# Kernel optimization log

Hardware: AMD Instinct MI355X
Metric: run time of the kernel (lower is better)

## Reference

```python
import jax, jax.numpy as jnp
import numpy as np


def setup_inputs() -> dict:
    key = jax.random.key(0)
    ks = jax.random.split(key, 6)
    B, N1, N2 = 4, 16384, 4096
    C1, C2 = 128, 256
    H1, H2 = 256, 128
    Cin = C1 + C2  # 384
    return {
        "xyz1": jax.random.normal(ks[0], (B, N1, 3), dtype=jnp.float32),
        "xyz2": jax.random.normal(ks[1], (B, N2, 3), dtype=jnp.float32),
        "features1": jax.random.normal(ks[2], (B, N1, C1), dtype=jnp.float32),
        "features2": jax.random.normal(ks[3], (B, N2, C2), dtype=jnp.float32),
        "W1": jax.random.normal(ks[4], (Cin, H1), dtype=jnp.float32) * (1.0 / np.sqrt(Cin)),
        "b1": jnp.zeros((H1,), dtype=jnp.float32),
        "W2": jax.random.normal(ks[5], (H1, H2), dtype=jnp.float32) * (1.0 / np.sqrt(H1)),
        "b2": jnp.zeros((H2,), dtype=jnp.float32),
    }


def reference(xyz1, xyz2, features1, features2, W1, b1, W2, b2):
    # Pairwise squared distances: [B, N1, N2]
    diff = xyz1[:, :, None, :] - xyz2[:, None, :, :]
    dist = jnp.sum(diff * diff, axis=-1)
    # 3 smallest distances (tf.argsort ascending, take first 3)
    neg_d3, idx = jax.lax.top_k(-dist, 3)          # idx: [B, N1, 3]
    d3 = jnp.maximum(-neg_d3, 1e-10)
    w = 1.0 / d3
    w = w / jnp.sum(w, axis=-1, keepdims=True)      # [B, N1, 3]
    # Gather features2 at the 3-NN indices per batch: [B, N1, 3, C2]
    gathered = jax.vmap(lambda f, i: f[i])(features2, idx)
    interp = jnp.sum(gathered * w[..., None], axis=2)  # [B, N1, C2]
    new_features = jnp.concatenate([interp, features1], axis=-1)  # [B, N1, C1+C2]
    # Pointwise MLP (Dense + ReLU, no BN)
    h = jax.nn.relu(jnp.einsum("bnc,ch->bnh", new_features, W1) + b1)
    out = jax.nn.relu(jnp.einsum("bnh,ho->bno", h, W2) + b2)
    return out
```

## Files before the change

kernel.cpp:

```cpp
#include <hip/hip_runtime.h>
#include <hip/hip_bf16.h>

typedef __bf16 bf16_t;
typedef __attribute__((ext_vector_type(8))) __bf16 bf16x8;
typedef __attribute__((ext_vector_type(4))) __bf16 bf16x4;
typedef __attribute__((ext_vector_type(4))) float f32x4;

#define N1 16384
#define N2 4096
#define C1 128
#define C2 256
#define CIN 384
#define HD1 256
#define HD2 128
#define BDIM 4
#define CHUNK 512
#define NCHUNK 8
#define NCAND 24

__global__ void prep_w(const float* __restrict__ W1, const float* __restrict__ W2,
                       const float* __restrict__ f2,
                       bf16_t* __restrict__ W1t, bf16_t* __restrict__ W2t,
                       bf16_t* __restrict__ f2bf) {
  int tid = blockIdx.x * 256 + threadIdx.x;
  if (tid < CIN * HD1) {
    int k = tid / HD1, n = tid % HD1;
    W1t[n * CIN + k] = (bf16_t)W1[tid];
  }
  if (tid < HD1 * HD2) {
    int k = tid / HD2, n = tid % HD2;
    W2t[n * HD1 + k] = (bf16_t)W2[tid];
  }
  const float4* s4 = (const float4*)f2;
  float4 a = s4[2 * (size_t)tid], b = s4[2 * (size_t)tid + 1];
  bf16x8 o;
  o[0] = (bf16_t)a.x; o[1] = (bf16_t)a.y; o[2] = (bf16_t)a.z; o[3] = (bf16_t)a.w;
  o[4] = (bf16_t)b.x; o[5] = (bf16_t)b.y; o[6] = (bf16_t)b.z; o[7] = (bf16_t)b.w;
  *(bf16x8*)(f2bf + (size_t)tid * 8) = o;
}

__global__ __launch_bounds__(256) void knn_chunk(
    const float* __restrict__ xyz1, const float* __restrict__ xyz2,
    float* __restrict__ candd, int* __restrict__ candj) {
  int b  = blockIdx.y;
  int ck = blockIdx.z;
  int i  = blockIdx.x * 256 + threadIdx.x;
  const float* p = xyz1 + ((size_t)b * N1 + i) * 3;
  float px = p[0], py = p[1], pz = p[2];

  const float* x2b = xyz2 + ((size_t)b * N2 + (size_t)ck * CHUNK) * 3;

  float d0 = 3.4e38f, d1 = 3.4e38f, d2 = 3.4e38f;
  int   j0 = 0, j1 = 0, j2 = 0;

  for (int j = 0; j < CHUNK; j += 16) {
    float c[48];
    const float4* q = (const float4*)(x2b + 3 * j);
#pragma unroll
    for (int t = 0; t < 12; ++t) {
      float4 v = q[t];
      c[4 * t + 0] = v.x; c[4 * t + 1] = v.y; c[4 * t + 2] = v.z; c[4 * t + 3] = v.w;
    }
#pragma unroll
    for (int u = 0; u < 16; ++u) {
      float dx = __fsub_rn(c[3 * u + 0], px);
      float dy = __fsub_rn(c[3 * u + 1], py);
      float dz = __fsub_rn(c[3 * u + 2], pz);
      float d = __fadd_rn(__fadd_rn(__fmul_rn(dx, dx), __fmul_rn(dy, dy)),
                          __fmul_rn(dz, dz));
      int jj = j + u;
      if (d < d2) {
        bool lt0 = d < d0, lt1 = d < d1;
        j2 = lt1 ? j1 : jj;
        j1 = lt0 ? j0 : (lt1 ? jj : j1);
        j0 = lt0 ? jj : j0;
        d2 = __builtin_amdgcn_fmed3f(d, d1, d2);
        d1 = __builtin_amdgcn_fmed3f(d, d0, d1);
        d0 = fminf(d, d0);
      }
    }
  }
  size_t qb = ((size_t)b * N1 + i) * NCAND + (size_t)ck * 3;
  int jbase = ck * CHUNK;
  candd[qb + 0] = d0; candd[qb + 1] = d1; candd[qb + 2] = d2;
  candj[qb + 0] = j0 + jbase; candj[qb + 1] = j1 + jbase; candj[qb + 2] = j2 + jbase;
}

__global__ __launch_bounds__(256) void knn_merge(
    const float* __restrict__ candd, const int* __restrict__ candj,
    float* __restrict__ wq, int* __restrict__ iq) {
  int q = blockIdx.x * 256 + threadIdx.x;
  const float* cd = candd + (size_t)q * NCAND;
  const int*   cj = candj + (size_t)q * NCAND;
  float d0 = 3.4e38f, d1 = 3.4e38f, d2 = 3.4e38f;
  int   j0 = 0, j1 = 0, j2 = 0;
#pragma unroll
  for (int c = 0; c < NCAND; ++c) {
    float d = cd[c]; int j = cj[c];
    bool p0 = d < d0, p1 = d < d1, p2 = d < d2;
    j2 = p1 ? j1 : (p2 ? j : j2);
    j1 = p0 ? j0 : (p1 ? j : j1);
    j0 = p0 ? j : j0;
    d2 = __builtin_amdgcn_fmed3f(d, d1, d2);
    d1 = __builtin_amdgcn_fmed3f(d, d0, d1);
    d0 = fminf(d, d0);
  }
  d0 = fmaxf(d0, 1e-10f); d1 = fmaxf(d1, 1e-10f); d2 = fmaxf(d2, 1e-10f);
  float w0 = 1.0f / d0, w1 = 1.0f / d1, w2 = 1.0f / d2;
  float ws = w0 + w1 + w2;
  wq[q * 3 + 0] = w0 / ws; wq[q * 3 + 1] = w1 / ws; wq[q * 3 + 2] = w2 / ws;
  iq[q * 3 + 0] = j0; iq[q * 3 + 1] = j1; iq[q * 3 + 2] = j2;
}

__global__ __launch_bounds__(256, 2) void interp_gemm1(
    const float* __restrict__ f1, const bf16_t* __restrict__ f2b_,
    const float* __restrict__ wq, const int* __restrict__ iq,
    const bf16_t* __restrict__ W1t, const float* __restrict__ b1,
    bf16_t* __restrict__ Hbuf) {
  __shared__ __align__(16) bf16_t As[128 * 32];
  __shared__ __align__(16) bf16_t Bs[4 * 256 * 8];
  int tid  = threadIdx.x;
  int wv   = tid >> 6, ln = tid & 63;
  int quad = ln >> 4, lm = ln & 15;
  long row0 = (long)blockIdx.x * 128;

  int srow = tid >> 1;
  int sh   = tid & 1;
  long q = row0 + srow;
  int  b = (int)(q >> 14);
  float u0 = wq[q * 3 + 0], u1 = wq[q * 3 + 1], u2 = wq[q * 3 + 2];
  const bf16_t* f2bb = f2b_ + (size_t)b * N2 * C2;
  const bf16_t* r0 = f2bb + (size_t)iq[q * 3 + 0] * C2;
  const bf16_t* r1 = f2bb + (size_t)iq[q * 3 + 1] * C2;
  const bf16_t* r2 = f2bb + (size_t)iq[q * 3 + 2] * C2;
  const float* f1r = f1 + (size_t)q * C1;
  bf16_t* asd = As + srow * 32 + sh * 16;

  int wm = (wv >> 1) * 64, wn = (wv & 1) * 128;
  f32x4 acc[4][8] = {};

  bf16x8 g0a, g0b, g1a, g1b, g2a, g2b;
  float4 gf[4];
  {
    int cb = sh * 16;
    g0a = *(const bf16x8*)(r0 + cb); g0b = *(const bf16x8*)(r0 + cb + 8);
    g1a = *(const bf16x8*)(r1 + cb); g1b = *(const bf16x8*)(r1 + cb + 8);
    g2a = *(const bf16x8*)(r2 + cb); g2b = *(const bf16x8*)(r2 + cb + 8);
  }

  for (int ks = 0; ks < 12; ++ks) {
    int kb = ks * 32;
#pragma unroll
    for (int s = 0; s < 4; ++s) {
      __builtin_amdgcn_global_load_lds(
          (const __attribute__((address_space(1))) void*)(
              W1t + (size_t)(wv * 64 + ln) * CIN + kb + s * 8),
          (__attribute__((address_space(3))) void*)(Bs + s * 2048 + wv * 512),
          16, 0, 0);
    }
    bf16x8 o[2];
    if (ks < 8) {
#pragma unroll
      for (int e = 0; e < 8; ++e) {
        o[0][e] = (bf16_t)(u0 * (float)g0a[e] + u1 * (float)g1a[e] +
                           u2 * (float)g2a[e]);
        o[1][e] = (bf16_t)(u0 * (float)g0b[e] + u1 * (float)g1b[e] +
                           u2 * (float)g2b[e]);
      }
    } else {
#pragma unroll
      for (int c4 = 0; c4 < 4; ++c4) {
        float4 g = gf[c4];
        int oi = c4 >> 1, off = (c4 & 1) * 4;
        o[oi][off + 0] = (bf16_t)g.x;
        o[oi][off + 1] = (bf16_t)g.y;
        o[oi][off + 2] = (bf16_t)g.z;
        o[oi][off + 3] = (bf16_t)g.w;
      }
    }
    *(bf16x8*)(asd) = o[0];
    *(bf16x8*)(asd + 8) = o[1];
    __syncthreads();

    if (ks < 7) {
      int cb = (ks + 1) * 32 + sh * 16;
      g0a = *(const bf16x8*)(r0 + cb); g0b = *(const bf16x8*)(r0 + cb + 8);
      g1a = *(const bf16x8*)(r1 + cb); g1b = *(const bf16x8*)(r1 + cb + 8);
      g2a = *(const bf16x8*)(r2 + cb); g2b = *(const bf16x8*)(r2 + cb + 8);
    } else if (ks < 11) {
      int cf = (ks - 7) * 32 + sh * 16;
#pragma unroll
      for (int c4 = 0; c4 < 4; ++c4)
        gf[c4] = *(const float4*)(f1r + cf + c4 * 4);
    }

    bf16x8 af[4];
#pragma unroll
    for (int mi = 0; mi < 4; ++mi)
      af[mi] = *(const bf16x8*)(As + (wm + mi * 16 + lm) * 32 + quad * 8);
#pragma unroll
    for (int nh = 0; nh < 2; ++nh) {
      bf16x8 bfr[4];
#pragma unroll
      for (int nn = 0; nn < 4; ++nn)
        bfr[nn] = *(const bf16x8*)(Bs + quad * 2048 + (wn + (nh * 4 + nn) * 16 + lm) * 8);
#pragma unroll
      for (int mi = 0; mi < 4; ++mi)
#pragma unroll
        for (int nn = 0; nn < 4; ++nn)
          acc[mi][nh * 4 + nn] = __builtin_amdgcn_mfma_f32_16x16x32_bf16(
              af[mi], bfr[nn], acc[mi][nh * 4 + nn], 0, 0, 0);
    }
    __syncthreads();
  }

#pragma unroll
  for (int mi = 0; mi < 4; ++mi)
#pragma unroll
    for (int ni = 0; ni < 8; ++ni) {
      int col = wn + ni * 16 + lm;
      float bv = b1[col];
#pragma unroll
      for (int r = 0; r < 4; ++r) {
        long rowg = row0 + wm + mi * 16 + quad * 4 + r;
        float v = acc[mi][ni][r] + bv;
        v = fmaxf(v, 0.0f);
        Hbuf[rowg * HD1 + col] = (bf16_t)v;
      }
    }
}

template <bool OUT_BF16>
__global__ __launch_bounds__(256) void gemm_bt(
    const bf16_t* __restrict__ A, const bf16_t* __restrict__ Bt,
    const float* __restrict__ bias, void* __restrict__ Cout,
    int M, int N, int K) {
  __shared__ __align__(16) bf16_t As[128 * 32];
  __shared__ __align__(16) bf16_t Bs[128 * 32];
  int tid  = threadIdx.x;
  int wv   = tid >> 6, ln = tid & 63;
  int quad = ln >> 4, lm = ln & 15;
  long row0 = (long)blockIdx.x * 128;
  int  col0 = blockIdx.y * 128;
  const bf16_t* Ab = A + row0 * K;
  const bf16_t* Bb = Bt + (long)col0 * K;
  f32x4 acc[4][4] = {};
  int wm = (wv >> 1) * 64, wn = (wv & 1) * 64;

  for (int k0 = 0; k0 < K; k0 += 32) {
#pragma unroll
    for (int t = 0; t < 2; ++t) {
      int c = t * 256 + tid;
      int r = c >> 2, kc = (c & 3) << 3;
      __builtin_amdgcn_global_load_lds(
          (const __attribute__((address_space(1))) void*)(Ab + (long)r * K + k0 + kc),
          (__attribute__((address_space(3))) void*)(As + (t * 256 + wv * 64) * 8),
          16, 0, 0);
      __builtin_amdgcn_global_load_lds(
          (const __attribute__((address_space(1))) void*)(Bb + (long)r * K + k0 + kc),
          (__attribute__((address_space(3))) void*)(Bs + (t * 256 + wv * 64) * 8),
          16, 0, 0);
    }
    __syncthreads();
    bf16x8 af[4], bfr[4];
#pragma unroll
    for (int mi = 0; mi < 4; ++mi)
      af[mi] = *(const bf16x8*)(As + (wm + mi * 16 + lm) * 32 + quad * 8);
#pragma unroll
    for (int ni = 0; ni < 4; ++ni)
      bfr[ni] = *(const bf16x8*)(Bs + (wn + ni * 16 + lm) * 32 + quad * 8);
#pragma unroll
    for (int mi = 0; mi < 4; ++mi)
#pragma unroll
      for (int ni = 0; ni < 4; ++ni)
        acc[mi][ni] = __builtin_amdgcn_mfma_f32_16x16x32_bf16(af[mi], bfr[ni],
                                                              acc[mi][ni], 0, 0, 0);
    __syncthreads();
  }

#pragma unroll
  for (int mi = 0; mi < 4; ++mi)
#pragma unroll
    for (int ni = 0; ni < 4; ++ni) {
      int col = col0 + wn + ni * 16 + lm;
      float bv = bias[col];
#pragma unroll
      for (int r = 0; r < 4; ++r) {
        long rowg = row0 + wm + mi * 16 + quad * 4 + r;
        float v = acc[mi][ni][r] + bv;
        v = fmaxf(v, 0.0f);
        if (OUT_BF16) ((bf16_t*)Cout)[rowg * N + col] = (bf16_t)v;
        else          ((float*)Cout)[rowg * N + col]  = v;
      }
    }
}

extern "C" void kernel_launch(void* const* d_in, const int* in_sizes, int n_in,
                              void* d_out, int out_size, void* d_ws, size_t ws_size,
                              hipStream_t stream) {
  const float* xyz1 = (const float*)d_in[0];
  const float* xyz2 = (const float*)d_in[1];
  const float* f1   = (const float*)d_in[2];
  const float* f2   = (const float*)d_in[3];
  const float* W1   = (const float*)d_in[4];
  const float* b1   = (const float*)d_in[5];
  const float* W2   = (const float*)d_in[6];
  const float* b2   = (const float*)d_in[7];
  float* out = (float*)d_out;

  const size_t NQ = (size_t)BDIM * N1;
  char* ws = (char*)d_ws;
  bf16_t* W1t = (bf16_t*)ws;
  bf16_t* W2t = (bf16_t*)(ws + (256 << 10));
  float*  wq  = (float*)(ws + (512 << 10));
  int*    iq  = (int*)(ws + (1536 << 10));
  bf16_t* f2bf = (bf16_t*)(ws + (2560 << 10));
  char*   hb  = ws + (2560 << 10) + NQ * CIN * 2;
  bf16_t* Hbuf  = (bf16_t*)hb;
  float*  candd = (float*)hb;
  int*    candj = (int*)(hb + NQ * NCAND * 4);

  prep_w<<<dim3(2048), dim3(256), 0, stream>>>(W1, W2, f2, W1t, W2t, f2bf);
  knn_chunk<<<dim3(N1 / 256, BDIM, NCHUNK), dim3(256), 0, stream>>>(
      xyz1, xyz2, candd, candj);
  knn_merge<<<dim3(NQ / 256), dim3(256), 0, stream>>>(candd, candj, wq, iq);
  interp_gemm1<<<dim3(NQ / 128), dim3(256), 0, stream>>>(
      f1, f2bf, wq, iq, W1t, b1, Hbuf);
  gemm_bt<false><<<dim3(NQ / 128, HD2 / 128), dim3(256), 0, stream>>>(
      Hbuf, W2t, b2, (void*)out, NQ, HD2, HD1);
}
```

Baseline: 245.0 us.

## Fuse kNN merge, interpolation, and both MLP layers into one tail kernel

Merges the knn_merge, interp_gemm1 and gemm_bt kernels into a single fused_tail kernel working on 64-row tiles. The top-3 merge results stay in shared memory, and the hidden activations are kept in swizzled LDS instead of going through a global Hbuf. This removes two kernel launches and the global round trip of H and the weight/index arrays. In exchange the M tile is smaller, so each block reloads the full W1 and W2 from global. The larger LDS footprint (about 52KB) may also limit occupancy.

Measured after the change: 263.5 us. 1.08x slower.

```diff
diff --git a/kernel.cpp b/kernel.cpp
--- a/kernel.cpp
+++ b/kernel.cpp
@@ -3,7 +3,6 @@
 
 typedef __bf16 bf16_t;
 typedef __attribute__((ext_vector_type(8))) __bf16 bf16x8;
-typedef __attribute__((ext_vector_type(4))) __bf16 bf16x4;
 typedef __attribute__((ext_vector_type(4))) float f32x4;
 
 #define N1 16384
@@ -86,66 +85,71 @@
   candj[qb + 0] = j0 + jbase; candj[qb + 1] = j1 + jbase; candj[qb + 2] = j2 + jbase;
 }
 
-__global__ __launch_bounds__(256) void knn_merge(
+__global__ __launch_bounds__(256, 3) void fused_tail(
+    const float* __restrict__ f1, const bf16_t* __restrict__ f2b_,
     const float* __restrict__ candd, const int* __restrict__ candj,
-    float* __restrict__ wq, int* __restrict__ iq) {
-  int q = blockIdx.x * 256 + threadIdx.x;
-  const float* cd = candd + (size_t)q * NCAND;
-  const int*   cj = candj + (size_t)q * NCAND;
-  float d0 = 3.4e38f, d1 = 3.4e38f, d2 = 3.4e38f;
-  int   j0 = 0, j1 = 0, j2 = 0;
-#pragma unroll
-  for (int c = 0; c < NCAND; ++c) {
-    float d = cd[c]; int j = cj[c];
-    bool p0 = d < d0, p1 = d < d1, p2 = d < d2;
-    j2 = p1 ? j1 : (p2 ? j : j2);
-    j1 = p0 ? j0 : (p1 ? j : j1);
-    j0 = p0 ? j : j0;
-    d2 = __builtin_amdgcn_fmed3f(d, d1, d2);
-    d1 = __builtin_amdgcn_fmed3f(d, d0, d1);
-    d0 = fminf(d, d0);
-  }
-  d0 = fmaxf(d0, 1e-10f); d1 = fmaxf(d1, 1e-10f); d2 = fmaxf(d2, 1e-10f);
-  float w0 = 1.0f / d0, w1 = 1.0f / d1, w2 = 1.0f / d2;
-  float ws = w0 + w1 + w2;
-  wq[q * 3 + 0] = w0 / ws; wq[q * 3 + 1] = w1 / ws; wq[q * 3 + 2] = w2 / ws;
-  iq[q * 3 + 0] = j0; iq[q * 3 + 1] = j1; iq[q * 3 + 2] = j2;
-}
-
-__global__ __launch_bounds__(256, 2) void interp_gemm1(
-    const float* __restrict__ f1, const bf16_t* __restrict__ f2b_,
-    const float* __restrict__ wq, const int* __restrict__ iq,
     const bf16_t* __restrict__ W1t, const float* __restrict__ b1,
-    bf16_t* __restrict__ Hbuf) {
-  __shared__ __align__(16) bf16_t As[128 * 32];
-  __shared__ __align__(16) bf16_t Bs[4 * 256 * 8];
-  int tid  = threadIdx.x;
-  int wv   = tid >> 6, ln = tid & 63;
-  int quad = ln >> 4, lm = ln & 15;
-  long row0 = (long)blockIdx.x * 128;
-
-  int srow = tid >> 1;
-  int sh   = tid & 1;
+    const bf16_t* __restrict__ W2t, const float* __restrict__ b2,
+    float* __restrict__ out) {
+  __shared__ __align__(16) char smem[53248];
+  bf16_t* As  = (bf16_t*)smem;
+  bf16_t* Bs  = (bf16_t*)(smem + 4096);
+  bf16_t* Bs2 = (bf16_t*)smem;
+  char*   hs  = smem + 20480;
+  float*  mw  = (float*)(smem + 20480);
+  int*    mj  = (int*)(smem + 20480 + 768);
+
+  int tid = threadIdx.x;
+  int wv = tid >> 6, ln = tid & 63, quad = ln >> 4, lm = ln & 15;
+  long row0 = (long)blockIdx.x * 64;
+
+  if (tid < 64) {
+    size_t q = row0 + tid;
+    const float* cd = candd + q * NCAND;
+    const int*   cj = candj + q * NCAND;
+    float d0 = 3.4e38f, d1 = 3.4e38f, d2 = 3.4e38f;
+    int   j0 = 0, j1 = 0, j2 = 0;
+#pragma unroll
+    for (int c = 0; c < NCAND; ++c) {
+      float d = cd[c]; int j = cj[c];
+      bool p0 = d < d0, p1 = d < d1, p2 = d < d2;
+      j2 = p1 ? j1 : (p2 ? j : j2);
+      j1 = p0 ? j0 : (p1 ? j : j1);
+      j0 = p0 ? j : j0;
+      d2 = __builtin_amdgcn_fmed3f(d, d1, d2);
+      d1 = __builtin_amdgcn_fmed3f(d, d0, d1);
+      d0 = fminf(d, d0);
+    }
+    d0 = fmaxf(d0, 1e-10f); d1 = fmaxf(d1, 1e-10f); d2 = fmaxf(d2, 1e-10f);
+    float w0 = 1.0f / d0, w1 = 1.0f / d1, w2 = 1.0f / d2;
+    float ws = w0 + w1 + w2;
+    mw[tid * 3 + 0] = w0 / ws; mw[tid * 3 + 1] = w1 / ws; mw[tid * 3 + 2] = w2 / ws;
+    mj[tid * 3 + 0] = j0; mj[tid * 3 + 1] = j1; mj[tid * 3 + 2] = j2;
+  }
+  __syncthreads();
+
+  int srow = tid >> 2, sh = tid & 3;
   long q = row0 + srow;
   int  b = (int)(q >> 14);
-  float u0 = wq[q * 3 + 0], u1 = wq[q * 3 + 1], u2 = wq[q * 3 + 2];
+  float u0 = mw[srow * 3 + 0], u1 = mw[srow * 3 + 1], u2 = mw[srow * 3 + 2];
   const bf16_t* f2bb = f2b_ + (size_t)b * N2 * C2;
-  const bf16_t* r0 = f2bb + (size_t)iq[q * 3 + 0] * C2;
-  const bf16_t* r1 = f2bb + (size_t)iq[q * 3 + 1] * C2;
-  const bf16_t* r2 = f2bb + (size_t)iq[q * 3 + 2] * C2;
+  const bf16_t* r0p = f2bb + (size_t)mj[srow * 3 + 0] * C2;
+  const bf16_t* r1p = f2bb + (size_t)mj[srow * 3 + 1] * C2;
+  const bf16_t* r2p = f2bb + (size_t)mj[srow * 3 + 2] * C2;
   const float* f1r = f1 + (size_t)q * C1;
-  bf16_t* asd = As + srow * 32 + sh * 16;
-
-  int wm = (wv >> 1) * 64, wn = (wv & 1) * 128;
-  f32x4 acc[4][8] = {};
-
-  bf16x8 g0a, g0b, g1a, g1b, g2a, g2b;
-  float4 gf[4];
+  bf16_t* asd = As + srow * 32 + sh * 8;
+  __syncthreads();
+
+  int wn = wv * 64;
+  f32x4 acc[4][4] = {};
+
+  bf16x8 g0, g1, g2;
+  float4 gfa, gfb;
   {
-    int cb = sh * 16;
-    g0a = *(const bf16x8*)(r0 + cb); g0b = *(const bf16x8*)(r0 + cb + 8);
-    g1a = *(const bf16x8*)(r1 + cb); g1b = *(const bf16x8*)(r1 + cb + 8);
-    g2a = *(const bf16x8*)(r2 + cb); g2b = *(const bf16x8*)(r2 + cb + 8);
+    int cb = sh * 8;
+    g0 = *(const bf16x8*)(r0p + cb);
+    g1 = *(const bf16x8*)(r1p + cb);
+    g2 = *(const bf16x8*)(r2p + cb);
   }
 
   for (int ks = 0; ks < 12; ++ks) {
@@ -158,117 +162,39 @@
           (__attribute__((address_space(3))) void*)(Bs + s * 2048 + wv * 512),
           16, 0, 0);
     }
-    bf16x8 o[2];
+    bf16x8 o;
     if (ks < 8) {
 #pragma unroll
-      for (int e = 0; e < 8; ++e) {
-        o[0][e] = (bf16_t)(u0 * (float)g0a[e] + u1 * (float)g1a[e] +
-                           u2 * (float)g2a[e]);
-        o[1][e] = (bf16_t)(u0 * (float)g0b[e] + u1 * (float)g1b[e] +
-                           u2 * (float)g2b[e]);
-      }
+      for (int e = 0; e < 8; ++e)
+        o[e] = (bf16_t)(u0 * (float)g0[e] + u1 * (float)g1[e] + u2 * (float)g2[e]);
     } else {
-#pragma unroll
-      for (int c4 = 0; c4 < 4; ++c4) {
-        float4 g = gf[c4];
-        int oi = c4 >> 1, off = (c4 & 1) * 4;
-        o[oi][off + 0] = (bf16_t)g.x;
-        o[oi][off + 1] = (bf16_t)g.y;
-        o[oi][off + 2] = (bf16_t)g.z;
-        o[oi][off + 3] = (bf16_t)g.w;
-      }
-    }
-    *(bf16x8*)(asd) = o[0];
-    *(bf16x8*)(asd + 8) = o[1];
+      o[0] = (bf16_t)gfa.x; o[1] = (bf16_t)gfa.y;
+      o[2] = (bf16_t)gfa.z; o[3] = (bf16_t)gfa.w;
+      o[4] = (bf16_t)gfb.x; o[5] = (bf16_t)gfb.y;
+      o[6] = (bf16_t)gfb.z; o[7] = (bf16_t)gfb.w;
+    }
+    *(bf16x8*)(asd) = o;
     __syncthreads();
 
     if (ks < 7) {
-      int cb = (ks + 1) * 32 + sh * 16;
-      g0a = *(const bf16x8*)(r0 + cb); g0b = *(const bf16x8*)(r0 + cb + 8);
-      g1a = *(const bf16x8*)(r1 + cb); g1b = *(const bf16x8*)(r1 + cb + 8);
-      g2a = *(const bf16x8*)(r2 + cb); g2b = *(const bf16x8*)(r2 + cb + 8);
+      int cb = (ks + 1) * 32 + sh * 8;
+      g0 = *(const bf16x8*)(r0p + cb);
+      g1 = *(const bf16x8*)(r1p + cb);
+      g2 = *(const bf16x8*)(r2p + cb);
     } else if (ks < 11) {
-      int cf = (ks - 7) * 32 + sh * 16;
-#pragma unroll
-      for (int c4 = 0; c4 < 4; ++c4)
-        gf[c4] = *(const float4*)(f1r + cf + c4 * 4);
+      int cf = (ks - 7) * 32 + sh * 8;
+      gfa = *(const float4*)(f1r + cf);
+      gfb = *(const float4*)(f1r + cf + 4);
     }
 
     bf16x8 af[4];
 #pragma unroll
     for (int mi = 0; mi < 4; ++mi)
-      af[mi] = *(const bf16x8*)(As + (wm + mi * 16 + lm) * 32 + quad * 8);
-#pragma unroll
-    for (int nh = 0; nh < 2; ++nh) {
-      bf16x8 bfr[4];
-#pragma unroll
-      for (int nn = 0; nn < 4; ++nn)
-        bfr[nn] = *(const bf16x8*)(Bs + quad * 2048 + (wn + (nh * 4 + nn) * 16 + lm) * 8);
-#pragma unroll
-      for (int mi = 0; mi < 4; ++mi)
-#pragma unroll
-        for (int nn = 0; nn < 4; ++nn)
-          acc[mi][nh * 4 + nn] = __builtin_amdgcn_mfma_f32_16x16x32_bf16(
-              af[mi], bfr[nn], acc[mi][nh * 4 + nn], 0, 0, 0);
-    }
-    __syncthreads();
-  }
-
-#pragma unroll
-  for (int mi = 0; mi < 4; ++mi)
-#pragma unroll
-    for (int ni = 0; ni < 8; ++ni) {
-      int col = wn + ni * 16 + lm;
-      float bv = b1[col];
-#pragma unroll
-      for (int r = 0; r < 4; ++r) {
-        long rowg = row0 + wm + mi * 16 + quad * 4 + r;
-        float v = acc[mi][ni][r] + bv;
-        v = fmaxf(v, 0.0f);
-        Hbuf[rowg * HD1 + col] = (bf16_t)v;
-      }
-    }
-}
-
-template <bool OUT_BF16>
-__global__ __launch_bounds__(256) void gemm_bt(
-    const bf16_t* __restrict__ A, const bf16_t* __restrict__ Bt,
-    const float* __restrict__ bias, void* __restrict__ Cout,
-    int M, int N, int K) {
-  __shared__ __align__(16) bf16_t As[128 * 32];
-  __shared__ __align__(16) bf16_t Bs[128 * 32];
-  int tid  = threadIdx.x;
-  int wv   = tid >> 6, ln = tid & 63;
-  int quad = ln >> 4, lm = ln & 15;
-  long row0 = (long)blockIdx.x * 128;
-  int  col0 = blockIdx.y * 128;
-  const bf16_t* Ab = A + row0 * K;
-  const bf16_t* Bb = Bt + (long)col0 * K;
-  f32x4 acc[4][4] = {};
-  int wm = (wv >> 1) * 64, wn = (wv & 1) * 64;
-
-  for (int k0 = 0; k0 < K; k0 += 32) {
-#pragma unroll
-    for (int t = 0; t < 2; ++t) {
-      int c = t * 256 + tid;
-      int r = c >> 2, kc = (c & 3) << 3;
-      __builtin_amdgcn_global_load_lds(
-          (const __attribute__((address_space(1))) void*)(Ab + (long)r * K + k0 + kc),
-          (__attribute__((address_space(3))) void*)(As + (t * 256 + wv * 64) * 8),
-          16, 0, 0);
-      __builtin_amdgcn_global_load_lds(
-          (const __attribute__((address_space(1))) void*)(Bb + (long)r * K + k0 + kc),
-          (__attribute__((address_space(3))) void*)(Bs + (t * 256 + wv * 64) * 8),
-          16, 0, 0);
-    }
-    __syncthreads();
-    bf16x8 af[4], bfr[4];
-#pragma unroll
-    for (int mi = 0; mi < 4; ++mi)
-      af[mi] = *(const bf16x8*)(As + (wm + mi * 16 + lm) * 32 + quad * 8);
+      af[mi] = *(const bf16x8*)(As + (mi * 16 + lm) * 32 + quad * 8);
+    bf16x8 bfr[4];
 #pragma unroll
     for (int ni = 0; ni < 4; ++ni)
-      bfr[ni] = *(const bf16x8*)(Bs + (wn + ni * 16 + lm) * 32 + quad * 8);
+      bfr[ni] = *(const bf16x8*)(Bs + quad * 2048 + (wn + ni * 16 + lm) * 8);
 #pragma unroll
     for (int mi = 0; mi < 4; ++mi)
 #pragma unroll
@@ -282,17 +208,58 @@
   for (int mi = 0; mi < 4; ++mi)
 #pragma unroll
     for (int ni = 0; ni < 4; ++ni) {
-      int col = col0 + wn + ni * 16 + lm;
-      float bv = bias[col];
+      int col = wn + ni * 16 + lm;
+      float bv = b1[col];
 #pragma unroll
       for (int r = 0; r < 4; ++r) {
-        long rowg = row0 + wm + mi * 16 + quad * 4 + r;
+        int row = mi * 16 + quad * 4 + r;
         float v = acc[mi][ni][r] + bv;
         v = fmaxf(v, 0.0f);
-        if (OUT_BF16) ((bf16_t*)Cout)[rowg * N + col] = (bf16_t)v;
-        else          ((float*)Cout)[rowg * N + col]  = v;
+        int byte = (row * 512 + col * 2) ^ ((row & 7) << 4);
+        *(bf16_t*)(hs + byte) = (bf16_t)v;
       }
     }
+  __syncthreads();
+
+  f32x4 acc2[8] = {};
+  for (int k0 = 0; k0 < HD1; k0 += 32) {
+#pragma unroll
+    for (int s = 0; s < 2; ++s) {
+      int idx = s * 256 + wv * 64 + ln;
+      __builtin_amdgcn_global_load_lds(
+          (const __attribute__((address_space(1))) void*)(
+              W2t + (size_t)(idx & 127) * HD1 + k0 + (idx >> 7) * 8),
+          (__attribute__((address_space(3))) void*)(Bs2 + (s * 256 + wv * 64) * 8),
+          16, 0, 0);
+    }
+    __syncthreads();
+
+    int hrow = wv * 16 + lm;
+    bf16x8 af2 = *(const bf16x8*)(
+        hs + ((hrow * 512 + (k0 + quad * 8) * 2) ^ ((lm & 7) << 4)));
+    bf16x8 bfr2[8];
+#pragma unroll
+    for (int ni = 0; ni < 8; ++ni)
+      bfr2[ni] = *(const bf16x8*)(Bs2 + (quad * 128 + ni * 16 + lm) * 8);
+#pragma unroll
+    for (int ni = 0; ni < 8; ++ni)
+      acc2[ni] = __builtin_amdgcn_mfma_f32_16x16x32_bf16(af2, bfr2[ni],
+                                                         acc2[ni], 0, 0, 0);
+    __syncthreads();
+  }
+
+#pragma unroll
+  for (int ni = 0; ni < 8; ++ni) {
+    int col = ni * 16 + lm;
+    float bv = b2[col];
+#pragma unroll
+    for (int r = 0; r < 4; ++r) {
+      long rowg = row0 + wv * 16 + quad * 4 + r;
+      float v = acc2[ni][r] + bv;
+      v = fmaxf(v, 0.0f);
+      out[rowg * HD2 + col] = v;
+    }
+  }
 }
 
 extern "C" void kernel_launch(void* const* d_in, const int* in_sizes, int n_in,
@@ -310,22 +277,15 @@
 
   const size_t NQ = (size_t)BDIM * N1;
   char* ws = (char*)d_ws;
-  bf16_t* W1t = (bf16_t*)ws;
-  bf16_t* W2t = (bf16_t*)(ws + (256 << 10));
-  float*  wq  = (float*)(ws + (512 << 10));
-  int*    iq  = (int*)(ws + (1536 << 10));
-  bf16_t* f2bf = (bf16_t*)(ws + (2560 << 10));
-  char*   hb  = ws + (2560 << 10) + NQ * CIN * 2;
-  bf16_t* Hbuf  = (bf16_t*)hb;
-  float*  candd = (float*)hb;
-  int*    candj = (int*)(hb + NQ * NCAND * 4);
+  bf16_t* W1t  = (bf16_t*)ws;
+  bf16_t* W2t  = (bf16_t*)(ws + (256 << 10));
+  bf16_t* f2bf = (bf16_t*)(ws + (512 << 10));
+  float*  candd = (float*)(ws + (10 << 20));
+  int*    candj = (int*)(ws + (17 << 20));
 
   prep_w<<<dim3(2048), dim3(256), 0, stream>>>(W1, W2, f2, W1t, W2t, f2bf);
   knn_chunk<<<dim3(N1 / 256, BDIM, NCHUNK), dim3(256), 0, stream>>>(
       xyz1, xyz2, candd, candj);
-  knn_merge<<<dim3(NQ / 256), dim3(256), 0, stream>>>(candd, candj, wq, iq);
-  interp_gemm1<<<dim3(NQ / 128), dim3(256), 0, stream>>>(
-      f1, f2bf, wq, iq, W1t, b1, Hbuf);
-  gemm_bt<false><<<dim3(NQ / 128, HD2 / 128), dim3(256), 0, stream>>>(
-      Hbuf, W2t, b2, (void*)out, NQ, HD2, HD1);
-}
+  fused_tail<<<dim3(NQ / 64), dim3(256), 0, stream>>>(
+      f1, f2bf, candd, candj, W1t, b1, W2t, b2, out);
+}
```
